# Kernel tuning notes

Measured on AMD Instinct MI355X. Metric: run time of the kernel, lower is better.

Reference implementation:

```python
import jax, jax.numpy as jnp
import numpy as np

N_GROUPS = 2048  # (d+1)//2 with d=4096


def setup_inputs() -> dict:
    key = jax.random.key(0)
    k1, k2, k3 = jax.random.split(key, 3)
    x = jax.random.normal(k1, (4096, 4096), dtype=jnp.float32)
    # Lloyd-Max style scalar codebook: sorted 16 levels (2^bits, bits=4)
    centroids = jnp.sort(jax.random.normal(k2, (16,), dtype=jnp.float32))
    # random planar rotations: angles ~ U[0, 2pi), stored as (cos, sin)
    angles = jax.random.uniform(k3, (N_GROUPS,), dtype=jnp.float32) * (2.0 * np.pi)
    rot2 = jnp.stack([jnp.cos(angles), jnp.sin(angles)], axis=-1)
    return {"x": x, "centroids": centroids, "rot2": rot2}


def reference(x, centroids, rot2):
    B, d = x.shape
    n_groups = rot2.shape[0]
    # --- quantize ---
    norms = jnp.clip(jnp.linalg.norm(x, axis=-1, keepdims=True), 1e-8)  # [B,1]
    x_unit = x / norms
    v = x_unit.reshape(B, n_groups, 2)
    c, s = rot2[:, 0], rot2[:, 1]  # [G]
    r0 = c * v[..., 0] - s * v[..., 1]
    r1 = s * v[..., 0] + c * v[..., 1]
    flat = jnp.stack([r0, r1], axis=-1).reshape(B, d)  # rotated coords [B,d]
    # per-scalar nearest-centroid search over n_levels
    indices = jnp.argmin(jnp.abs(flat[..., None] - centroids), axis=-1)  # [B,d]
    # --- dequantize ---
    q = centroids[indices].reshape(B, n_groups, 2)
    f0 = c * q[..., 0] + s * q[..., 1]   # inverse rotation
    f1 = -s * q[..., 0] + c * q[..., 1]
    x_hat = jnp.stack([f0, f1], axis=-1).reshape(B, d) * norms
    return x_hat, indices
```

## Files before the change

kernel.cpp:

```cpp
#include <hip/hip_runtime.h>


#define ROW_D     4096
#define BLOCK_T   256
#define F4_PER_T  4

__device__ __forceinline__ void quant_pair(
    float x0, float x1, float c, float s,
    float invf, float dnf, double invd,
    const float* __restrict__ cf, const float* __restrict__ mf,
    const float* __restrict__ cent,
    float& o0, float& o1, float& i0, float& i1)
{
    const float v0 = x0 * invf, v1 = x1 * invf;
    const float r0 = c * v0 - s * v1;
    const float r1 = s * v0 + c * v1;

    int a = 0, b = 0;
    float q0 = cf[0], q1 = cf[0];
    float m0 = 3.4e38f, m1 = 3.4e38f;
#pragma unroll
    for (int j = 0; j < 15; ++j) {
        const float t0 = r0 - mf[j];
        const float t1 = r1 - mf[j];
        const bool ca = t0 > 0.0f;
        const bool cb = t1 > 0.0f;
        a += ca ? 1 : 0;
        b += cb ? 1 : 0;
        q0 = ca ? cf[j + 1] : q0;
        q1 = cb ? cf[j + 1] : q1;
        m0 = fminf(m0, fabsf(t0));
        m1 = fminf(m1, fabsf(t1));
    }

    const float EPS = 1e-5f;
    if (m0 < EPS || m1 < EPS) {
        const double v0d = (double)x0 * invd;
        const double v1d = (double)x1 * invd;
        const double cd = (double)c, sd = (double)s;
        const double r0d = cd * v0d - sd * v1d;
        const double r1d = sd * v0d + cd * v1d;
        a = 0; b = 0;
        double q0d = (double)cent[0], q1d = (double)cent[0];
#pragma unroll
        for (int j = 0; j < 15; ++j) {
            const double mj = 0.5 * ((double)cent[j] + (double)cent[j + 1]);
            const bool ca = r0d > mj;
            const bool cb = r1d > mj;
            a += ca ? 1 : 0;
            b += cb ? 1 : 0;
            q0d = ca ? (double)cent[j + 1] : q0d;
            q1d = cb ? (double)cent[j + 1] : q1d;
        }
        q0 = (float)q0d;
        q1 = (float)q1d;
    }

    const float f0 = c * q0 + s * q1;
    const float f1 = c * q1 - s * q0;
    o0 = f0 * dnf;
    o1 = f1 * dnf;
    i0 = (float)a;
    i1 = (float)b;
}

__global__ __launch_bounds__(BLOCK_T) void planar_quant_kernel(
    const float* __restrict__ x,
    const float* __restrict__ cent,
    const float* __restrict__ rot2,
    float* __restrict__ out_xhat,
    float* __restrict__ out_idx)
{
    const int row = blockIdx.x;
    const int t   = threadIdx.x;

    const float4* xr = (const float4*)(x + (size_t)row * ROW_D);

    float4 xa[F4_PER_T];
    double ss = 0.0;
#pragma unroll
    for (int i = 0; i < F4_PER_T; ++i) {
        float4 v = xr[t + BLOCK_T * i];
        xa[i] = v;
        ss += (double)v.x * (double)v.x;
        ss += (double)v.y * (double)v.y;
        ss += (double)v.z * (double)v.z;
        ss += (double)v.w * (double)v.w;
    }

#pragma unroll
    for (int off = 32; off > 0; off >>= 1)
        ss += __shfl_down(ss, off, 64);

    __shared__ double smem[5];
    const int wid = t >> 6;
    if ((t & 63) == 0) smem[wid] = ss;
    __syncthreads();
    if (t == 0) {
        double tot = smem[0] + smem[1] + smem[2] + smem[3];
        double n = sqrt(tot);
        smem[4] = (n < 1e-8) ? 1e-8 : n;
    }
    __syncthreads();
    const double dnd  = smem[4];
    const double invd = 1.0 / dnd;
    const float  dnf  = (float)dnd;
    const float  invf = (float)invd;

    float cf[16];
#pragma unroll
    for (int j = 0; j < 16; ++j) cf[j] = cent[j];
    float mf[15];
#pragma unroll
    for (int j = 0; j < 15; ++j) mf[j] = 0.5f * (cf[j] + cf[j + 1]);

    const float4* rr = (const float4*)rot2;
    float4* xo = (float4*)(out_xhat + (size_t)row * ROW_D);
    float4* io = (float4*)(out_idx  + (size_t)row * ROW_D);

#pragma unroll
    for (int i = 0; i < F4_PER_T; ++i) {
        const int f = t + BLOCK_T * i;
        const float4 xv = xa[i];
        const float4 rv = rr[f];
        float4 ov, iv;
        quant_pair(xv.x, xv.y, rv.x, rv.y, invf, dnf, invd, cf, mf, cent,
                   ov.x, ov.y, iv.x, iv.y);
        quant_pair(xv.z, xv.w, rv.z, rv.w, invf, dnf, invd, cf, mf, cent,
                   ov.z, ov.w, iv.z, iv.w);
        xo[f] = ov;
        io[f] = iv;
    }
}

extern "C" void kernel_launch(void* const* d_in, const int* in_sizes, int n_in,
                              void* d_out, int out_size, void* d_ws, size_t ws_size,
                              hipStream_t stream) {
    const float* x    = (const float*)d_in[0];
    const float* cent = (const float*)d_in[1];
    const float* rot2 = (const float*)d_in[2];

    const int d = in_sizes[2];
    const int B = in_sizes[0] / d;

    float* out  = (float*)d_out;
    float* xhat = out;
    float* idxo = out + (size_t)B * d;

    planar_quant_kernel<<<B, BLOCK_T, 0, stream>>>(x, cent, rot2, xhat, idxo);
}
```

Baseline: 190.3 us.

## Use shared-memory centroid/midpoint table and nontemporal loads/stores

```diff
diff --git a/kernel.cpp b/kernel.cpp
--- a/kernel.cpp
+++ b/kernel.cpp
@@ -5,36 +5,36 @@
 #define BLOCK_T   256
 #define F4_PER_T  4
 
-__device__ __forceinline__ void quant_pair(
+typedef float f32x4 __attribute__((ext_vector_type(4)));
+
+struct QP { float o0, o1, i0, i1; };
+
+__device__ __forceinline__ QP quant_pair(
     float x0, float x1, float c, float s,
     float invf, float dnf, double invd,
-    const float* __restrict__ cf, const float* __restrict__ mf,
-    const float* __restrict__ cent,
-    float& o0, float& o1, float& i0, float& i1)
+    const float* __restrict__ mf,
+    const float2* __restrict__ w2,
+    const float* __restrict__ cent)
 {
     const float v0 = x0 * invf, v1 = x1 * invf;
     const float r0 = c * v0 - s * v1;
     const float r1 = s * v0 + c * v1;
 
     int a = 0, b = 0;
-    float q0 = cf[0], q1 = cf[0];
-    float m0 = 3.4e38f, m1 = 3.4e38f;
 #pragma unroll
     for (int j = 0; j < 15; ++j) {
-        const float t0 = r0 - mf[j];
-        const float t1 = r1 - mf[j];
-        const bool ca = t0 > 0.0f;
-        const bool cb = t1 > 0.0f;
-        a += ca ? 1 : 0;
-        b += cb ? 1 : 0;
-        q0 = ca ? cf[j + 1] : q0;
-        q1 = cb ? cf[j + 1] : q1;
-        m0 = fminf(m0, fabsf(t0));
-        m1 = fminf(m1, fabsf(t1));
+        a += (r0 > mf[j]) ? 1 : 0;
+        b += (r1 > mf[j]) ? 1 : 0;
     }
 
+    const float2 pa0 = w2[a],     pa1 = w2[a + 1];
+    const float2 pb0 = w2[b],     pb1 = w2[b + 1];
+    float q0 = pa0.y, q1 = pb0.y;
+
     const float EPS = 1e-5f;
-    if (m0 < EPS || m1 < EPS) {
+    const float g0 = fminf(r0 - pa0.x, pa1.x - r0);
+    const float g1 = fminf(r1 - pb0.x, pb1.x - r1);
+    if (g0 < EPS || g1 < EPS) {
         const double v0d = (double)x0 * invd;
         const double v1d = (double)x1 * invd;
         const double cd = (double)c, sd = (double)s;
@@ -56,12 +56,12 @@
         q1 = (float)q1d;
     }
 
-    const float f0 = c * q0 + s * q1;
-    const float f1 = c * q1 - s * q0;
-    o0 = f0 * dnf;
-    o1 = f1 * dnf;
-    i0 = (float)a;
-    i1 = (float)b;
+    QP r;
+    r.o0 = (c * q0 + s * q1) * dnf;
+    r.o1 = (c * q1 - s * q0) * dnf;
+    r.i0 = (float)a;
+    r.i1 = (float)b;
+    return r;
 }
 
 __global__ __launch_bounds__(BLOCK_T) void planar_quant_kernel(
@@ -74,13 +74,13 @@
     const int row = blockIdx.x;
     const int t   = threadIdx.x;
 
-    const float4* xr = (const float4*)(x + (size_t)row * ROW_D);
+    const f32x4* xr = (const f32x4*)(x + (size_t)row * ROW_D);
 
-    float4 xa[F4_PER_T];
+    f32x4 xa[F4_PER_T];
     double ss = 0.0;
 #pragma unroll
     for (int i = 0; i < F4_PER_T; ++i) {
-        float4 v = xr[t + BLOCK_T * i];
+        f32x4 v = __builtin_nontemporal_load(&xr[t + BLOCK_T * i]);
         xa[i] = v;
         ss += (double)v.x * (double)v.x;
         ss += (double)v.y * (double)v.y;
@@ -93,8 +93,23 @@
         ss += __shfl_down(ss, off, 64);
 
     __shared__ double smem[5];
+    __shared__ float2 w2[18];
     const int wid = t >> 6;
     if ((t & 63) == 0) smem[wid] = ss;
+
+    float cf[16];
+#pragma unroll
+    for (int j = 0; j < 16; ++j) cf[j] = cent[j];
+    float mf[15];
+#pragma unroll
+    for (int j = 0; j < 15; ++j) mf[j] = 0.5f * (cf[j] + cf[j + 1]);
+
+    if (t < 17) {
+        float md_lo = (t == 0)  ? -3.0e38f : 0.5f * (cf[t - 1] + cf[t]);
+        float cd_t  = (t < 16)  ? cf[t] : 0.0f;
+        w2[t] = make_float2(md_lo, cd_t);
+        if (t == 16) w2[16].x = 3.0e38f;
+    }
     __syncthreads();
     if (t == 0) {
         double tot = smem[0] + smem[1] + smem[2] + smem[3];
@@ -107,29 +122,22 @@
     const float  dnf  = (float)dnd;
     const float  invf = (float)invd;
 
-    float cf[16];
-#pragma unroll
-    for (int j = 0; j < 16; ++j) cf[j] = cent[j];
-    float mf[15];
-#pragma unroll
-    for (int j = 0; j < 15; ++j) mf[j] = 0.5f * (cf[j] + cf[j + 1]);
-
     const float4* rr = (const float4*)rot2;
-    float4* xo = (float4*)(out_xhat + (size_t)row * ROW_D);
-    float4* io = (float4*)(out_idx  + (size_t)row * ROW_D);
+    f32x4* xo = (f32x4*)(out_xhat + (size_t)row * ROW_D);
+    f32x4* io = (f32x4*)(out_idx  + (size_t)row * ROW_D);
 
 #pragma unroll
     for (int i = 0; i < F4_PER_T; ++i) {
         const int f = t + BLOCK_T * i;
-        const float4 xv = xa[i];
+        const f32x4 xv = xa[i];
         const float4 rv = rr[f];
-        float4 ov, iv;
-        quant_pair(xv.x, xv.y, rv.x, rv.y, invf, dnf, invd, cf, mf, cent,
-                   ov.x, ov.y, iv.x, iv.y);
-        quant_pair(xv.z, xv.w, rv.z, rv.w, invf, dnf, invd, cf, mf, cent,
-                   ov.z, ov.w, iv.z, iv.w);
-        xo[f] = ov;
-        io[f] = iv;
+        const QP lo = quant_pair(xv.x, xv.y, rv.x, rv.y, invf, dnf, invd, mf, w2, cent);
+        const QP hi = quant_pair(xv.z, xv.w, rv.z, rv.w, invf, dnf, invd, mf, w2, cent);
+        f32x4 ov, iv;
+        ov.x = lo.o0; ov.y = lo.o1; ov.z = hi.o0; ov.w = hi.o1;
+        iv.x = lo.i0; iv.y = lo.i1; iv.z = hi.i0; iv.w = hi.i1;
+        __builtin_nontemporal_store(ov, &xo[f]);
+        __builtin_nontemporal_store(iv, &io[f]);
     }
 }
 
```

After: 186.9 us. No clear change (-1.8%).
